# Kernel optimization log

Measured on AMD Instinct MI355X. Metric: run time of the kernel, lower is better.

Reference implementation:

```python
import jax, jax.numpy as jnp
import numpy as np

LN_EPS = 1e-5

def _gru_layer(x, W_ih, W_hh, b_ih, b_hh):
    # x: [B,S,Din]; W_ih: [3H,Din]; W_hh: [3H,H]; biases: [3H]
    B = x.shape[0]
    H = W_hh.shape[1]
    # Precompute input-side gate projections for all timesteps (one big GEMM).
    gx = jnp.einsum('bsd,gd->bsg', x, W_ih) + b_ih  # [B,S,3H]
    Whh_T = W_hh.T  # [H,3H]

    def step(h, gx_t):
        gh = h @ Whh_T + b_hh                     # [B,3H]
        xr, xz, xn = jnp.split(gx_t, 3, axis=-1)
        hr, hz, hn = jnp.split(gh, 3, axis=-1)
        r = jax.nn.sigmoid(xr + hr)
        z = jax.nn.sigmoid(xz + hz)
        n = jnp.tanh(xn + r * hn)
        h_new = (1.0 - z) * n + z * h
        return h_new, h_new

    h0 = jnp.zeros((B, H), dtype=x.dtype)
    h_last, ys = jax.lax.scan(step, h0, jnp.swapaxes(gx, 0, 1))  # ys: [S,B,H]
    return jnp.swapaxes(ys, 0, 1), h_last


def setup_inputs() -> dict:
    key = jax.random.key(0)
    ks = jax.random.split(key, 12)
    B, S, D, H = 256, 512, 64, 256
    L = 3
    s_in = 1.0 / np.sqrt(H)
    return {
        'x': jax.random.normal(ks[0], (B, S, D), dtype=jnp.float32),
        'W_ih0': jax.random.uniform(ks[1], (3 * H, D), jnp.float32, -s_in, s_in),
        'W_ih_rest': jax.random.uniform(ks[2], (L - 1, 3 * H, H), jnp.float32, -s_in, s_in),
        'W_hh': jax.random.uniform(ks[3], (L, 3 * H, H), jnp.float32, -s_in, s_in),
        'b_ih': jax.random.uniform(ks[4], (L, 3 * H), jnp.float32, -s_in, s_in),
        'b_hh': jax.random.uniform(ks[5], (L, 3 * H), jnp.float32, -s_in, s_in),
        'ln_gamma': jnp.ones((H,), jnp.float32),
        'ln_beta': jnp.zeros((H,), jnp.float32),
        'W1': jax.random.uniform(ks[6], (32, H), jnp.float32, -s_in, s_in),
        'b1': jax.random.uniform(ks[7], (32,), jnp.float32, -s_in, s_in),
        'W2': jax.random.uniform(ks[8], (1, 32), jnp.float32, -1 / np.sqrt(32), 1 / np.sqrt(32)),
        'b2': jax.random.uniform(ks[9], (1,), jnp.float32, -1 / np.sqrt(32), 1 / np.sqrt(32)),
    }


def reference(x, W_ih0, W_ih_rest, W_hh, b_ih, b_hh, ln_gamma, ln_beta, W1, b1, W2, b2):
    # Multi-layer GRU (batch_first), eval mode (dropout inactive).
    h = x
    L = W_hh.shape[0]
    h_last = None
    for l in range(L):
        W_ih_l = W_ih0 if l == 0 else W_ih_rest[l - 1]
        h, h_last = _gru_layer(h, W_ih_l, W_hh[l], b_ih[l], b_hh[l])
    last = h_last  # == out[:, -1, :]  [B,H]
    # LayerNorm
    mu = jnp.mean(last, axis=-1, keepdims=True)
    var = jnp.mean(jnp.square(last - mu), axis=-1, keepdims=True)
    last = (last - mu) * jax.lax.rsqrt(var + LN_EPS) * ln_gamma + ln_beta
    # MLP head
    hdn = jax.nn.relu(last @ W1.T + b1)
    pred = hdn @ W2.T + b2  # [B,1]
    return pred[:, 0]
```

## Files before the change

kernel.cpp:

```cpp
#include <hip/hip_runtime.h>
#include <stdint.h>

#define B_  256
#define S_  512
#define D_  64
#define H_  256
#define G3_ 768

typedef __attribute__((ext_vector_type(8))) short s8v;
typedef __attribute__((ext_vector_type(4))) short s4v;
typedef __attribute__((ext_vector_type(4))) float f4v;
typedef __attribute__((ext_vector_type(4))) float f4r;

#define MF(a, b, c) __builtin_amdgcn_mfma_f32_16x16x32_bf16((a), (b), (c), 0, 0, 0)

__device__ __forceinline__ unsigned short f2bf(float x) {
  unsigned u = __float_as_uint(x);
  unsigned r = (u + 0x7fffu + ((u >> 16) & 1u)) >> 16;
  return (unsigned short)r;
}
__device__ __forceinline__ float bf2f(unsigned short s) {
  return __uint_as_float(((unsigned)s) << 16);
}
__device__ __forceinline__ float sigm(float x) {
  return __builtin_amdgcn_rcpf(1.f + __expf(-x));
}
__device__ __forceinline__ float tanh_f(float x) {
  return 1.f - 2.f * __builtin_amdgcn_rcpf(1.f + __expf(2.f * x));
}

__global__ __launch_bounds__(256) void pack_bf16(
    const float* __restrict__ src, unsigned short* __restrict__ dst, int n8)
{
  const int i = blockIdx.x * 256 + threadIdx.x;
  if (i >= n8) return;
  const float4 f0 = *(const float4*)(src + (size_t)i * 8);
  const float4 f1 = *(const float4*)(src + (size_t)i * 8 + 4);
  unsigned short h[8] = { f2bf(f0.x), f2bf(f0.y), f2bf(f0.z), f2bf(f0.w),
                          f2bf(f1.x), f2bf(f1.y), f2bf(f1.z), f2bf(f1.w) };
  *(s8v*)&dst[(size_t)i * 8] = *(s8v*)h;
}

__global__ __launch_bounds__(64) void pack_whh(
    const float* __restrict__ Whh, unsigned short* __restrict__ Whp,
    const float* __restrict__ bih, const float* __restrict__ bhh,
    float* __restrict__ bias2)
{
  const int gti = blockIdx.x, kc = blockIdx.y, lane = threadIdx.x;
  const int rowp = gti * 16 + (lane & 15);
  const int k0  = kc * 32 + (lane >> 4) * 8;
  const float* src = &Whh[(size_t)rowp * H_ + k0];
  unsigned short hi8[8];
  #pragma unroll
  for (int s = 0; s < 8; ++s) hi8[s] = f2bf(src[s]);
  const size_t o = ((size_t)(gti * 8 + kc) * 64 + lane) * 8;
  *(s8v*)&Whp[o] = *(s8v*)hi8;

  if (gti == 0 && kc == 0) {
    #pragma unroll
    for (int i = 0; i < 12; ++i) {
      int g = i * 64 + lane;
      bias2[g] = bih[g] + (g < 512 ? bhh[g] : 0.f);
    }
  }
}

__global__ __launch_bounds__(1024, 4) void fused_step(
    int s, int CH, int chsh, int cpl,
    const float* __restrict__ x, unsigned short* __restrict__ ybf,
    const unsigned short* __restrict__ wihp,
    const unsigned short* __restrict__ Whp, const float* __restrict__ bhh_all,
    const float* __restrict__ bias2, unsigned short* __restrict__ gxbase,
    float* __restrict__ hbuf)
{
  const int tid = threadIdx.x;
  const int wid = tid >> 6, lane = tid & 63;
  const int fr = lane & 15, fq = lane >> 4;
  const size_t gx_elems = (size_t)B_ * CH * G3_;

  extern __shared__ unsigned short lds_[];

  if (blockIdx.x < 48) {
    const int l = blockIdx.x >> 4;
    const int c = s - 2 * l;
    if (c < 0 || c >= cpl) return;

    const unsigned short* Whp_s = Whp + (size_t)l * G3_ * H_;
    const float* bhh_s = bhh_all + (size_t)l * G3_;
    float* hb = hbuf + (size_t)l * B_ * H_;
    const unsigned short* gx_r = gxbase + (size_t)(2 * l + (c & 1)) * gx_elems;
    const int t0s = c * CH;
    const int lastL = (l == 2) ? 1 : 0;

    unsigned short* WhN  = lds_;
    unsigned short* Abuf = lds_ + 65536;

    const int bid = blockIdx.x & 15;
    const int b0  = bid * 16;
    const int bb  = fr;

    const s8v* WhpV = (const s8v*)Whp_s;

    s8v whr[8], whz[8];
    #pragma unroll
    for (int kc = 0; kc < 8; ++kc) {
      whr[kc] = WhpV[((     wid) * 8 + kc) * 64 + lane];
      whz[kc] = WhpV[((16 + wid) * 8 + kc) * 64 + lane];
    }
    #pragma unroll
    for (int kc = 0; kc < 8; ++kc) {
      s8v v = WhpV[((32 + wid) * 8 + kc) * 64 + lane];
      *(s8v*)&WhN[(wid * 8 + kc) * 512 + lane * 8] = v;
    }

    const int u0 = 16 * wid + 4 * fq;
    const f4r bhn4 = *(const f4r*)&bhh_s[2 * H_ + u0];

    f4r hn4 = {0.f, 0.f, 0.f, 0.f};
    if (t0s != 0) hn4 = *(const f4r*)&hb[(size_t)(b0 + bb) * H_ + u0];

    const int kcw  = wid >> 1;
    const int lp   = bb | (((2 * wid + (fq >> 1)) & 3) << 4);
    const int eo   = (fq & 1) * 4;
    const int aoff = kcw * 512 + lp * 8 + eo;

    {
      s4v hh;
      #pragma unroll
      for (int j = 0; j < 4; ++j) hh[j] = (short)f2bf(hn4[j]);
      *(s4v*)&Abuf[aoff] = hh;
    }

    const unsigned short* gb0 = gx_r + ((size_t)(b0 + bb) * CH) * G3_;
    s4v xr4 = *(const s4v*)(gb0 + u0);
    s4v xz4 = *(const s4v*)(gb0 + H_ + u0);
    s4v xn4 = *(const s4v*)(gb0 + 2 * H_ + u0);

    int cur = 0;
    for (int t = 0; t < CH; ++t) {
      __syncthreads();

      const int tn = (t + 1 < CH) ? t + 1 : t;
      const unsigned short* gbn = gx_r + ((size_t)(b0 + bb) * CH + tn) * G3_;
      s4v xr_n = *(const s4v*)(gbn + u0);
      s4v xz_n = *(const s4v*)(gbn + H_ + u0);
      s4v xn_n = *(const s4v*)(gbn + 2 * H_ + u0);

      f4v accR = {}, accZ = {}, accN = {};
      #pragma unroll
      for (int kc = 0; kc < 8; ++kc) {
        s8v ahh = *(const s8v*)&Abuf[cur * 4096 + kc * 512 + lane * 8];
        s8v wn  = *(const s8v*)&WhN[(wid * 8 + kc) * 512 + lane * 8];
        accR = MF(whr[kc], ahh, accR);
        accZ = MF(whz[kc], ahh, accZ);
        accN = MF(wn,      ahh, accN);
      }

      #pragma unroll
      for (int i = 0; i < 4; ++i) {
        const float r = sigm(bf2f((unsigned short)xr4[i]) + accR[i]);
        const float z = sigm(bf2f((unsigned short)xz4[i]) + accZ[i]);
        const float n = tanh_f(bf2f((unsigned short)xn4[i]) + r * (accN[i] + bhn4[i]));
        hn4[i] = (1.f - z) * n + z * hn4[i];
      }
      s4v hh;
      #pragma unroll
      for (int j = 0; j < 4; ++j) hh[j] = (short)f2bf(hn4[j]);
      if (!lastL) {
        __builtin_nontemporal_store(
            hh, (s4v*)&ybf[((size_t)(b0 + bb) * S_ + (t0s + t)) * H_ + u0]);
      }
      *(s4v*)&Abuf[(cur ^ 1) * 4096 + aoff] = hh;
      xr4 = xr_n; xz4 = xz_n; xn4 = xn_n;
      cur ^= 1;
    }

    *(f4r*)&hb[(size_t)(b0 + bb) * H_ + u0] = hn4;

  } else {
    const int g = blockIdx.x - 48;
    const int per = CH * 12;
    const int l = g / per;
    if (l >= 3) return;
    const int c2 = s + 1 - 2 * l;
    if (c2 < 0 || c2 >= cpl) return;

    const int gidx  = g % per;
    const int mtile = gidx / 12, gtile = gidx % 12;
    const int r0 = mtile * 256, g0 = gtile * 64;

    const int    K   = (l == 0) ? D_ : H_;
    const unsigned short* Wp =
        (l == 0) ? wihp : (wihp + 49152 + (size_t)(l - 1) * 196608);
    const float* b2g = bias2 + l * 768;
    unsigned short* gx_w = gxbase + (size_t)(2 * l + (c2 & 1)) * gx_elems;
    const int t0g = c2 * CH;

    unsigned short* Ah  = lds_;
    unsigned short* Wh  = lds_ + 10240;
    unsigned short* gxs = lds_ + 12800;

    const int row = tid >> 2;
    const int ks  = (tid & 3) * 8;
    const int r = r0 + row;
    const int rg = ((r >> chsh) * S_) + t0g + (r & (CH - 1));

    f4v acc[4] = {};

    for (int k0 = 0; k0 < K; k0 += 32) {
      s8v aval;
      if (l == 0) {
        const float* apf = x + (size_t)rg * D_ + k0 + ks;
        float4 f0 = *(const float4*)(apf);
        float4 f1 = *(const float4*)(apf + 4);
        unsigned short a8[8] = { f2bf(f0.x), f2bf(f0.y), f2bf(f0.z), f2bf(f0.w),
                                 f2bf(f1.x), f2bf(f1.y), f2bf(f1.z), f2bf(f1.w) };
        aval = *(s8v*)a8;
      } else {
        aval = *(const s8v*)(ybf + (size_t)rg * H_ + k0 + ks);
      }
      s8v wval;
      if (tid < 256)
        wval = *(const s8v*)(Wp + (size_t)(g0 + row) * K + k0 + ks);
      __syncthreads();
      *(s8v*)&Ah[row * 40 + ks] = aval;
      if (tid < 256) *(s8v*)&Wh[row * 40 + ks] = wval;
      __syncthreads();

      s8v a_hi = *(const s8v*)&Ah[(16 * wid + fr) * 40 + fq * 8];
      #pragma unroll
      for (int c = 0; c < 4; ++c) {
        s8v b_hi = *(const s8v*)&Wh[(c * 16 + fr) * 40 + fq * 8];
        acc[c] = MF(a_hi, b_hi, acc[c]);
      }
    }

    #pragma unroll
    for (int c = 0; c < 4; ++c) {
      const float bi = b2g[g0 + c * 16 + fr];
      #pragma unroll
      for (int i = 0; i < 4; ++i)
        gxs[(wid * 16 + fq * 4 + i) * 64 + c * 16 + fr] = f2bf(acc[c][i] + bi);
    }
    __syncthreads();
    {
      const int srow = tid >> 2, soff = (tid & 3) * 16;
      s8v v0 = *(const s8v*)&gxs[srow * 64 + soff];
      s8v v1 = *(const s8v*)&gxs[srow * 64 + soff + 8];
      unsigned short* gp = gx_w + (size_t)(r0 + srow) * G3_ + g0 + soff;
      *(s8v*)gp = v0;
      *(s8v*)(gp + 8) = v1;
    }
  }
}

__global__ __launch_bounds__(64) void head_kernel(
    const float* __restrict__ hlast, const float* __restrict__ lng,
    const float* __restrict__ lnb, const float* __restrict__ W1,
    const float* __restrict__ b1, const float* __restrict__ W2,
    const float* __restrict__ b2, float* __restrict__ out)
{
  const int b = blockIdx.x;
  const int lane = threadIdx.x;
  float4 v = *(const float4*)&hlast[(size_t)b * H_ + lane * 4];
  float s = v.x + v.y + v.z + v.w;
  #pragma unroll
  for (int m = 32; m > 0; m >>= 1) s += __shfl_xor(s, m, 64);
  const float mu = s * (1.f / 256.f);
  const float dx = v.x - mu, dy = v.y - mu, dz = v.z - mu, dw = v.w - mu;
  float q = dx*dx + dy*dy + dz*dz + dw*dw;
  #pragma unroll
  for (int m = 32; m > 0; m >>= 1) q += __shfl_xor(q, m, 64);
  const float rstd = rsqrtf(q * (1.f / 256.f) + 1e-5f);

  __shared__ float ln[256];
  const int i4 = lane * 4;
  ln[i4 + 0] = dx * rstd * lng[i4 + 0] + lnb[i4 + 0];
  ln[i4 + 1] = dy * rstd * lng[i4 + 1] + lnb[i4 + 1];
  ln[i4 + 2] = dz * rstd * lng[i4 + 2] + lnb[i4 + 2];
  ln[i4 + 3] = dw * rstd * lng[i4 + 3] + lnb[i4 + 3];
  __syncthreads();

  float hd = 0.f;
  if (lane < 32) {
    const float* w = W1 + (size_t)lane * H_;
    float a = 0.f;
    for (int k = 0; k < H_; ++k) a += ln[k] * w[k];
    a += b1[lane];
    hd = fmaxf(a, 0.f) * W2[lane];
  }
  #pragma unroll
  for (int m = 16; m > 0; m >>= 1) hd += __shfl_xor(hd, m, 64);
  if (lane == 0) out[b] = hd + b2[0];
}

extern "C" void kernel_launch(void* const* d_in, const int* in_sizes, int n_in,
                              void* d_out, int out_size, void* d_ws, size_t ws_size,
                              hipStream_t stream)
{
  const float* x     = (const float*)d_in[0];
  const float* W_ih0 = (const float*)d_in[1];
  const float* W_ihr = (const float*)d_in[2];
  const float* W_hh  = (const float*)d_in[3];
  const float* b_ih  = (const float*)d_in[4];
  const float* b_hh  = (const float*)d_in[5];
  const float* lng   = (const float*)d_in[6];
  const float* lnb   = (const float*)d_in[7];
  const float* W1    = (const float*)d_in[8];
  const float* b1    = (const float*)d_in[9];
  const float* W2    = (const float*)d_in[10];
  const float* b2    = (const float*)d_in[11];
  float* out = (float*)d_out;

  const size_t ybf_elems  = (size_t)B_ * S_ * H_;
  const size_t wihp_elems = 49152 + 2 * 196608;
  const size_t h_elems    = (size_t)B_ * H_;
  const size_t whp_elems  = (size_t)G3_ * H_;

  int CH = 64;
  while (CH > 8) {
    size_t need = ybf_elems * 2 + wihp_elems * 2
                + 6 * (size_t)B_ * CH * G3_ * 2
                + (3 * h_elems + 3 * 768) * 4
                + 3 * whp_elems * 2 + 8192;
    if (need <= ws_size) break;
    CH >>= 1;
  }
  const int chsh = __builtin_ctz((unsigned)CH);
  const size_t gx_elems = (size_t)B_ * CH * G3_;
  const int cpl = S_ / CH;

  unsigned short* ybf    = (unsigned short*)d_ws;
  unsigned short* wihp   = ybf + ybf_elems;
  unsigned short* gxbase = wihp + wihp_elems;
  float* hbuf = (float*)(gxbase + 6 * gx_elems);
  unsigned short* Whp = (unsigned short*)(hbuf + 3 * h_elems);
  float* bias2 = (float*)(Whp + 3 * whp_elems);

  const size_t lds_bytes = 131072 + 16384;
  const int grid = 48 + 3 * CH * 12;

  pack_bf16<<<(49152 / 8 + 255) / 256, 256, 0, stream>>>(W_ih0, wihp, 49152 / 8);
  pack_bf16<<<(393216 / 8 + 255) / 256, 256, 0, stream>>>(
      W_ihr, wihp + 49152, 393216 / 8);
  for (int l = 0; l < 3; ++l) {
    pack_whh<<<dim3(48, 8), 64, 0, stream>>>(
        W_hh + (size_t)l * G3_ * H_, Whp + (size_t)l * whp_elems,
        b_ih + (size_t)l * G3_, b_hh + (size_t)l * G3_, bias2 + l * 768);
  }

  for (int s = -1; s <= cpl + 3; ++s) {
    fused_step<<<grid, 1024, lds_bytes, stream>>>(
        s, CH, chsh, cpl, x, ybf, wihp, Whp, b_hh, bias2, gxbase, hbuf);
  }

  head_kernel<<<256, 64, 0, stream>>>(hbuf + 2 * h_elems, lng, lnb,
                                      W1, b1, W2, b2, out);
}
```

Measured before the change: 1.524 ms.

## Replace per-step kernel launches with a persistent cooperative kernel using flag sync

```diff
diff --git a/kernel.cpp b/kernel.cpp
--- a/kernel.cpp
+++ b/kernel.cpp
@@ -27,6 +27,16 @@
 }
 __device__ __forceinline__ float tanh_f(float x) {
   return 1.f - 2.f * __builtin_amdgcn_rcpf(1.f + __expf(2.f * x));
+}
+
+__device__ __forceinline__ void waitFlag(unsigned* p, unsigned target) {
+  while (__hip_atomic_load(p, __ATOMIC_RELAXED, __HIP_MEMORY_SCOPE_AGENT) < target)
+    __builtin_amdgcn_s_sleep(2);
+  (void)__hip_atomic_load(p, __ATOMIC_ACQUIRE, __HIP_MEMORY_SCOPE_AGENT);
+}
+__device__ __forceinline__ void postFlag(unsigned* p) {
+  __threadfence();
+  __hip_atomic_fetch_add(p, 1u, __ATOMIC_RELEASE, __HIP_MEMORY_SCOPE_AGENT);
 }
 
 __global__ __launch_bounds__(256) void pack_bf16(
@@ -65,31 +75,29 @@
   }
 }
 
-__global__ __launch_bounds__(1024, 4) void fused_step(
-    int s, int CH, int chsh, int cpl,
+__global__ __launch_bounds__(1024, 4) void persist_k(
+    int CH, int chsh, int cpl,
     const float* __restrict__ x, unsigned short* __restrict__ ybf,
     const unsigned short* __restrict__ wihp,
     const unsigned short* __restrict__ Whp, const float* __restrict__ bhh_all,
     const float* __restrict__ bias2, unsigned short* __restrict__ gxbase,
-    float* __restrict__ hbuf)
+    float* __restrict__ hbuf, unsigned* __restrict__ gemm_done,
+    unsigned* __restrict__ scan_done)
 {
   const int tid = threadIdx.x;
   const int wid = tid >> 6, lane = tid & 63;
   const int fr = lane & 15, fq = lane >> 4;
   const size_t gx_elems = (size_t)B_ * CH * G3_;
+  const unsigned NTILES = (unsigned)(CH * 12);
 
   extern __shared__ unsigned short lds_[];
 
   if (blockIdx.x < 48) {
     const int l = blockIdx.x >> 4;
-    const int c = s - 2 * l;
-    if (c < 0 || c >= cpl) return;
 
     const unsigned short* Whp_s = Whp + (size_t)l * G3_ * H_;
     const float* bhh_s = bhh_all + (size_t)l * G3_;
     float* hb = hbuf + (size_t)l * B_ * H_;
-    const unsigned short* gx_r = gxbase + (size_t)(2 * l + (c & 1)) * gx_elems;
-    const int t0s = c * CH;
     const int lastL = (l == 2) ? 1 : 0;
 
     unsigned short* WhN  = lds_;
@@ -117,7 +125,6 @@
     const f4r bhn4 = *(const f4r*)&bhh_s[2 * H_ + u0];
 
     f4r hn4 = {0.f, 0.f, 0.f, 0.f};
-    if (t0s != 0) hn4 = *(const f4r*)&hb[(size_t)(b0 + bb) * H_ + u0];
 
     const int kcw  = wid >> 1;
     const int lp   = bb | (((2 * wid + (fq >> 1)) & 3) << 4);
@@ -131,70 +138,68 @@
       *(s4v*)&Abuf[aoff] = hh;
     }
 
-    const unsigned short* gb0 = gx_r + ((size_t)(b0 + bb) * CH) * G3_;
-    s4v xr4 = *(const s4v*)(gb0 + u0);
-    s4v xz4 = *(const s4v*)(gb0 + H_ + u0);
-    s4v xn4 = *(const s4v*)(gb0 + 2 * H_ + u0);
-
     int cur = 0;
-    for (int t = 0; t < CH; ++t) {
+    for (int c = 0; c < cpl; ++c) {
+      if (tid == 0) waitFlag(&gemm_done[l * cpl + c], NTILES);
       __syncthreads();
 
-      const int tn = (t + 1 < CH) ? t + 1 : t;
-      const unsigned short* gbn = gx_r + ((size_t)(b0 + bb) * CH + tn) * G3_;
-      s4v xr_n = *(const s4v*)(gbn + u0);
-      s4v xz_n = *(const s4v*)(gbn + H_ + u0);
-      s4v xn_n = *(const s4v*)(gbn + 2 * H_ + u0);
-
-      f4v accR = {}, accZ = {}, accN = {};
-      #pragma unroll
-      for (int kc = 0; kc < 8; ++kc) {
-        s8v ahh = *(const s8v*)&Abuf[cur * 4096 + kc * 512 + lane * 8];
-        s8v wn  = *(const s8v*)&WhN[(wid * 8 + kc) * 512 + lane * 8];
-        accR = MF(whr[kc], ahh, accR);
-        accZ = MF(whz[kc], ahh, accZ);
-        accN = MF(wn,      ahh, accN);
+      const unsigned short* gx_r = gxbase + (size_t)(2 * l + (c & 1)) * gx_elems;
+      const int t0s = c * CH;
+
+      const unsigned short* gb0 = gx_r + ((size_t)(b0 + bb) * CH) * G3_;
+      s4v xr4 = *(const s4v*)(gb0 + u0);
+      s4v xz4 = *(const s4v*)(gb0 + H_ + u0);
+      s4v xn4 = *(const s4v*)(gb0 + 2 * H_ + u0);
+
+      for (int t = 0; t < CH; ++t) {
+        __syncthreads();
+
+        const int tn = (t + 1 < CH) ? t + 1 : t;
+        const unsigned short* gbn = gx_r + ((size_t)(b0 + bb) * CH + tn) * G3_;
+        s4v xr_n = *(const s4v*)(gbn + u0);
+        s4v xz_n = *(const s4v*)(gbn + H_ + u0);
+        s4v xn_n = *(const s4v*)(gbn + 2 * H_ + u0);
+
+        f4v accR = {}, accZ = {}, accN = {};
+        #pragma unroll
+        for (int kc = 0; kc < 8; ++kc) {
+          s8v ahh = *(const s8v*)&Abuf[cur * 4096 + kc * 512 + lane * 8];
+          s8v wn  = *(const s8v*)&WhN[(wid * 8 + kc) * 512 + lane * 8];
+          accR = MF(whr[kc], ahh, accR);
+          accZ = MF(whz[kc], ahh, accZ);
+          accN = MF(wn,      ahh, accN);
+        }
+
+        #pragma unroll
+        for (int i = 0; i < 4; ++i) {
+          const float r = sigm(bf2f((unsigned short)xr4[i]) + accR[i]);
+          const float z = sigm(bf2f((unsigned short)xz4[i]) + accZ[i]);
+          const float n = tanh_f(bf2f((unsigned short)xn4[i]) + r * (accN[i] + bhn4[i]));
+          hn4[i] = (1.f - z) * n + z * hn4[i];
+        }
+        s4v hh;
+        #pragma unroll
+        for (int j = 0; j < 4; ++j) hh[j] = (short)f2bf(hn4[j]);
+        if (!lastL) {
+          *(s4v*)&ybf[((size_t)(b0 + bb) * S_ + (t0s + t)) * H_ + u0] = hh;
+        }
+        *(s4v*)&Abuf[(cur ^ 1) * 4096 + aoff] = hh;
+        xr4 = xr_n; xz4 = xz_n; xn4 = xn_n;
+        cur ^= 1;
       }
 
-      #pragma unroll
-      for (int i = 0; i < 4; ++i) {
-        const float r = sigm(bf2f((unsigned short)xr4[i]) + accR[i]);
-        const float z = sigm(bf2f((unsigned short)xz4[i]) + accZ[i]);
-        const float n = tanh_f(bf2f((unsigned short)xn4[i]) + r * (accN[i] + bhn4[i]));
-        hn4[i] = (1.f - z) * n + z * hn4[i];
-      }
-      s4v hh;
-      #pragma unroll
-      for (int j = 0; j < 4; ++j) hh[j] = (short)f2bf(hn4[j]);
-      if (!lastL) {
-        __builtin_nontemporal_store(
-            hh, (s4v*)&ybf[((size_t)(b0 + bb) * S_ + (t0s + t)) * H_ + u0]);
-      }
-      *(s4v*)&Abuf[(cur ^ 1) * 4096 + aoff] = hh;
-      xr4 = xr_n; xz4 = xz_n; xn4 = xn_n;
-      cur ^= 1;
+      __syncthreads();
+      if (tid == 0) postFlag(&scan_done[l * cpl + c]);
     }
 
     *(f4r*)&hb[(size_t)(b0 + bb) * H_ + u0] = hn4;
 
   } else {
-    const int g = blockIdx.x - 48;
-    const int per = CH * 12;
-    const int l = g / per;
-    if (l >= 3) return;
-    const int c2 = s + 1 - 2 * l;
-    if (c2 < 0 || c2 >= cpl) return;
-
-    const int gidx  = g % per;
-    const int mtile = gidx / 12, gtile = gidx % 12;
+    const int wkr = blockIdx.x - 48;
+    if (wkr >= (int)NTILES) return;
+
+    const int mtile = wkr / 12, gtile = wkr % 12;
     const int r0 = mtile * 256, g0 = gtile * 64;
-
-    const int    K   = (l == 0) ? D_ : H_;
-    const unsigned short* Wp =
-        (l == 0) ? wihp : (wihp + 49152 + (size_t)(l - 1) * 196608);
-    const float* b2g = bias2 + l * 768;
-    unsigned short* gx_w = gxbase + (size_t)(2 * l + (c2 & 1)) * gx_elems;
-    const int t0g = c2 * CH;
 
     unsigned short* Ah  = lds_;
     unsigned short* Wh  = lds_ + 10240;
@@ -202,54 +207,96 @@
 
     const int row = tid >> 2;
     const int ks  = (tid & 3) * 8;
-    const int r = r0 + row;
-    const int rg = ((r >> chsh) * S_) + t0g + (r & (CH - 1));
-
-    f4v acc[4] = {};
-
-    for (int k0 = 0; k0 < K; k0 += 32) {
-      s8v aval;
-      if (l == 0) {
-        const float* apf = x + (size_t)rg * D_ + k0 + ks;
-        float4 f0 = *(const float4*)(apf);
-        float4 f1 = *(const float4*)(apf + 4);
-        unsigned short a8[8] = { f2bf(f0.x), f2bf(f0.y), f2bf(f0.z), f2bf(f0.w),
-                                 f2bf(f1.x), f2bf(f1.y), f2bf(f1.z), f2bf(f1.w) };
-        aval = *(s8v*)a8;
-      } else {
-        aval = *(const s8v*)(ybf + (size_t)rg * H_ + k0 + ks);
+
+    for (int s = 0; s <= cpl + 3; ++s) {
+      for (int l = 0; l < 3; ++l) {
+        const int c = s - 2 * l;
+        if (c < 0 || c >= cpl) continue;
+
+        if (tid == 0) {
+          if (l > 0)  waitFlag(&scan_done[(l - 1) * cpl + c], 16u);
+          if (c >= 2) waitFlag(&scan_done[l * cpl + (c - 2)], 16u);
+        }
+        __syncthreads();
+
+        const int    K   = (l == 0) ? D_ : H_;
+        const unsigned short* Wp =
+            (l == 0) ? wihp : (wihp + 49152 + (size_t)(l - 1) * 196608);
+        const float* b2g = bias2 + l * 768;
+        unsigned short* gx_w = gxbase + (size_t)(2 * l + (c & 1)) * gx_elems;
+        const int t0g = c * CH;
+
+        const int r = r0 + row;
+        const int rg = ((r >> chsh) * S_) + t0g + (r & (CH - 1));
+
+        f4v acc[4] = {};
+
+        s8v aval, wval, avalN, wvalN;
+        {
+          if (l == 0) {
+            const float* apf = x + (size_t)rg * D_ + ks;
+            float4 f0 = *(const float4*)(apf);
+            float4 f1 = *(const float4*)(apf + 4);
+            unsigned short a8[8] = { f2bf(f0.x), f2bf(f0.y), f2bf(f0.z), f2bf(f0.w),
+                                     f2bf(f1.x), f2bf(f1.y), f2bf(f1.z), f2bf(f1.w) };
+            aval = *(s8v*)a8;
+          } else {
+            aval = *(const s8v*)(ybf + (size_t)rg * H_ + ks);
+          }
+          if (tid < 256)
+            wval = *(const s8v*)(Wp + (size_t)(g0 + row) * K + ks);
+        }
+        for (int k0 = 0; k0 < K; k0 += 32) {
+          __syncthreads();
+          *(s8v*)&Ah[row * 40 + ks] = aval;
+          if (tid < 256) *(s8v*)&Wh[row * 40 + ks] = wval;
+          if (k0 + 32 < K) {
+            const int kn = k0 + 32;
+            if (l == 0) {
+              const float* apf = x + (size_t)rg * D_ + kn + ks;
+              float4 f0 = *(const float4*)(apf);
+              float4 f1 = *(const float4*)(apf + 4);
+              unsigned short a8[8] = { f2bf(f0.x), f2bf(f0.y), f2bf(f0.z), f2bf(f0.w),
+                                       f2bf(f1.x), f2bf(f1.y), f2bf(f1.z), f2bf(f1.w) };
+              avalN = *(s8v*)a8;
+            } else {
+              avalN = *(const s8v*)(ybf + (size_t)rg * H_ + kn + ks);
+            }
+            if (tid < 256)
+              wvalN = *(const s8v*)(Wp + (size_t)(g0 + row) * K + kn + ks);
+          }
+          __syncthreads();
+
+          s8v a_hi = *(const s8v*)&Ah[(16 * wid + fr) * 40 + fq * 8];
+          #pragma unroll
+          for (int cc = 0; cc < 4; ++cc) {
+            s8v b_hi = *(const s8v*)&Wh[(cc * 16 + fr) * 40 + fq * 8];
+            acc[cc] = MF(a_hi, b_hi, acc[cc]);
+          }
+          aval = avalN; wval = wvalN;
+        }
+
+        __syncthreads();
+        #pragma unroll
+        for (int cc = 0; cc < 4; ++cc) {
+          const float bi = b2g[g0 + cc * 16 + fr];
+          #pragma unroll
+          for (int i = 0; i < 4; ++i)
+            gxs[(wid * 16 + fq * 4 + i) * 72 + cc * 16 + fr] = f2bf(acc[cc][i] + bi);
+        }
+        __syncthreads();
+        {
+          const int srow = tid >> 2, soff = (tid & 3) * 16;
+          s8v v0 = *(const s8v*)&gxs[srow * 72 + soff];
+          s8v v1 = *(const s8v*)&gxs[srow * 72 + soff + 8];
+          unsigned short* gp = gx_w + (size_t)(r0 + srow) * G3_ + g0 + soff;
+          *(s8v*)gp = v0;
+          *(s8v*)(gp + 8) = v1;
+        }
+
+        __syncthreads();
+        if (tid == 0) postFlag(&gemm_done[l * cpl + c]);
       }
-      s8v wval;
-      if (tid < 256)
-        wval = *(const s8v*)(Wp + (size_t)(g0 + row) * K + k0 + ks);
-      __syncthreads();
-      *(s8v*)&Ah[row * 40 + ks] = aval;
-      if (tid < 256) *(s8v*)&Wh[row * 40 + ks] = wval;
-      __syncthreads();
-
-      s8v a_hi = *(const s8v*)&Ah[(16 * wid + fr) * 40 + fq * 8];
-      #pragma unroll
-      for (int c = 0; c < 4; ++c) {
-        s8v b_hi = *(const s8v*)&Wh[(c * 16 + fr) * 40 + fq * 8];
-        acc[c] = MF(a_hi, b_hi, acc[c]);
-      }
-    }
-
-    #pragma unroll
-    for (int c = 0; c < 4; ++c) {
-      const float bi = b2g[g0 + c * 16 + fr];
-      #pragma unroll
-      for (int i = 0; i < 4; ++i)
-        gxs[(wid * 16 + fq * 4 + i) * 64 + c * 16 + fr] = f2bf(acc[c][i] + bi);
-    }
-    __syncthreads();
-    {
-      const int srow = tid >> 2, soff = (tid & 3) * 16;
-      s8v v0 = *(const s8v*)&gxs[srow * 64 + soff];
-      s8v v1 = *(const s8v*)&gxs[srow * 64 + soff + 8];
-      unsigned short* gp = gx_w + (size_t)(r0 + srow) * G3_ + g0 + soff;
-      *(s8v*)gp = v0;
-      *(s8v*)(gp + 8) = v1;
     }
   }
 }
@@ -317,7 +364,7 @@
   const size_t h_elems    = (size_t)B_ * H_;
   const size_t whp_elems  = (size_t)G3_ * H_;
 
-  int CH = 64;
+  int CH = 16;
   while (CH > 8) {
     size_t need = ybf_elems * 2 + wihp_elems * 2
                 + 6 * (size_t)B_ * CH * G3_ * 2
@@ -336,9 +383,12 @@
   float* hbuf = (float*)(gxbase + 6 * gx_elems);
   unsigned short* Whp = (unsigned short*)(hbuf + 3 * h_elems);
   float* bias2 = (float*)(Whp + 3 * whp_elems);
+  unsigned* gemm_done = (unsigned*)(bias2 + 3 * 768);
+  unsigned* scan_done = gemm_done + 3 * cpl;
 
   const size_t lds_bytes = 131072 + 16384;
-  const int grid = 48 + 3 * CH * 12;
+
+  hipMemsetAsync(gemm_done, 0, 2 * 3 * (size_t)cpl * sizeof(unsigned), stream);
 
   pack_bf16<<<(49152 / 8 + 255) / 256, 256, 0, stream>>>(W_ih0, wihp, 49152 / 8);
   pack_bf16<<<(393216 / 8 + 255) / 256, 256, 0, stream>>>(
@@ -349,9 +399,22 @@
         b_ih + (size_t)l * G3_, b_hh + (size_t)l * G3_, bias2 + l * 768);
   }
 
-  for (int s = -1; s <= cpl + 3; ++s) {
-    fused_step<<<grid, 1024, lds_bytes, stream>>>(
-        s, CH, chsh, cpl, x, ybf, wihp, Whp, b_hh, bias2, gxbase, hbuf);
+  {
+    int CHa = CH, chsha = chsh, cpla = cpl;
+    const float* xa = x;
+    unsigned short* ybfa = ybf;
+    const unsigned short* wihpa = wihp;
+    const unsigned short* Whpa = Whp;
+    const float* bhha = b_hh;
+    const float* bias2a = bias2;
+    unsigned short* gxa = gxbase;
+    float* hbufa = hbuf;
+    unsigned* gda = gemm_done;
+    unsigned* sda = scan_done;
+    void* args[] = { &CHa, &chsha, &cpla, &xa, &ybfa, &wihpa, &Whpa, &bhha,
+                     &bias2a, &gxa, &hbufa, &gda, &sda };
+    hipLaunchCooperativeKernel((void*)persist_k, dim3(256), dim3(1024),
+                               args, (unsigned)lds_bytes, stream);
   }
 
   head_kernel<<<256, 64, 0, stream>>>(hbuf + 2 * h_elems, lng, lnb,
```

After: 2.487 ms. 63.3% more time.
